# Kernel optimization log

Hardware: AMD Instinct MI355X
Metric: run time of the kernel (lower is better)

The kernel has to match this reference:

```python
import jax, jax.numpy as jnp
import numpy as np

EPS = 1e-5

def setup_inputs() -> dict:
    key = jax.random.key(0)
    ks = jax.random.split(key, 10)
    B, N, D = 1, 20000, 256
    E, H = 320000, 8
    s = 1.0 / np.sqrt(D)
    return {
        "node_embeddings": jax.random.normal(ks[0], (B, N, D), jnp.float32),
        "edge_index": jax.random.randint(ks[1], (2, E), 0, N, jnp.int32),
        "edge_weights": jax.random.uniform(ks[2], (E,), jnp.float32),
        "Wq": jax.random.normal(ks[3], (D, D), jnp.float32) * s,
        "Wk": jax.random.normal(ks[4], (D, D), jnp.float32) * s,
        "Wv": jax.random.normal(ks[5], (D, D), jnp.float32) * s,
        "We": jax.random.normal(ks[6], (H,), jnp.float32),  # edge_encoder weight [num_heads,1] squeezed
        "Wo": jax.random.normal(ks[7], (D, D), jnp.float32) * s,
        "ln_g": jnp.ones((D,), jnp.float32),
        "ln_b": jnp.zeros((D,), jnp.float32),
    }

def reference(node_embeddings, edge_index, edge_weights, Wq, Wk, Wv, We, Wo, ln_g, ln_b):
    B, N, D = node_embeddings.shape
    H = We.shape[0]
    hd = D // H
    scale = 1.0 / np.sqrt(hd)
    residual = node_embeddings

    # projections -> [B, N, H, hd]
    Q = (node_embeddings @ Wq).reshape(B, N, H, hd)
    K = (node_embeddings @ Wk).reshape(B, N, H, hd)
    V = (node_embeddings @ Wv).reshape(B, N, H, hd)

    src = edge_index[0]
    tgt = edge_index[1]
    E = src.shape[0]

    # gather per edge, edge axis leading for segment ops: [E, B, H, hd]
    Q_e = jnp.moveaxis(Q[:, src], 1, 0)
    K_e = jnp.moveaxis(K[:, tgt], 1, 0)
    V_e = jnp.moveaxis(V[:, tgt], 1, 0)

    # per-edge scores [E, B, H]
    scores = (Q_e * K_e).sum(-1) * scale
    bias = edge_weights[:, None] * We[None, :]            # [E, H]
    scores = scores + bias[:, None, :]

    # scatter softmax grouped by source node
    m = jax.ops.segment_max(scores, src, num_segments=N)   # [N, B, H]
    p = jnp.exp(scores - m[src])
    denom = jax.ops.segment_sum(p, src, num_segments=N)    # [N, B, H]
    attn = p / denom[src]                                   # [E, B, H]

    # scatter-add weighted V -> [N, B, H, hd]
    weighted = attn[..., None] * V_e
    agg = jax.ops.segment_sum(weighted.reshape(E, -1), src, num_segments=N)
    agg = agg.reshape(N, B, H, hd)

    attn_out = jnp.moveaxis(agg, 0, 1).reshape(B, N, D)     # [B, N, D]
    out = attn_out @ Wo

    x = out + residual
    mu = x.mean(-1, keepdims=True)
    var = ((x - mu) ** 2).mean(-1, keepdims=True)
    return (x - mu) / jnp.sqrt(var + EPS) * ln_g + ln_b
```

## Files before the change

### kernel.cpp

```cpp
#include <hip/hip_runtime.h>
#include <hip/hip_bf16.h>

typedef __attribute__((ext_vector_type(8))) short short8;
typedef __attribute__((ext_vector_type(4))) short short4_t;
typedef __attribute__((ext_vector_type(4))) float f32x4;

#define CH 64

__device__ __forceinline__ ushort f2b(float f) {
  __hip_bfloat16 h = __float2bfloat16(f);
  return *reinterpret_cast<ushort*>(&h);
}
__device__ __forceinline__ float b2f(ushort u) {
  return __uint_as_float(((unsigned)u) << 16);
}
__device__ __forceinline__ void wave_lds_sync() {
  asm volatile("s_waitcnt lgkmcnt(0)" ::: "memory");
  __builtin_amdgcn_wave_barrier();
}

__global__ __launch_bounds__(256) void pre_kernel(
    const float* __restrict__ Wq, const float* __restrict__ Wk,
    const float* __restrict__ Wv, const float* __restrict__ Wo,
    ushort* __restrict__ Wt, const int* __restrict__ src,
    int* __restrict__ counts, int E) {
  __shared__ float L[32][33];
  int b = blockIdx.x;
  int t = threadIdx.x;
  if (b < 256) {
    int mat = b >> 6;
    int tile = b & 63;
    int tr = (tile >> 3) * 32;
    int tc = (tile & 7) * 32;
    const float* W = (mat == 0) ? Wq : (mat == 1) ? Wk : (mat == 2) ? Wv : Wo;
    int c = t & 31, r8 = t >> 5;
#pragma unroll
    for (int rr = 0; rr < 4; ++rr) {
      int r = r8 + rr * 8;
      L[r][c] = W[(size_t)(tr + r) * 256 + tc + c];
    }
    __syncthreads();
#pragma unroll
    for (int rr = 0; rr < 4; ++rr) {
      int cc = r8 + rr * 8;
      Wt[(size_t)(mat * 256 + tc + cc) * 256 + tr + c] = f2b(L[c][cc]);
    }
  } else {
    int e = (b - 256) * 256 + t;
    if (e < E) atomicAdd(&counts[src[e]], 1);
  }
}

__global__ __launch_bounds__(256) void gemm_scan(
    const float* __restrict__ X, const ushort* __restrict__ Wt,
    ushort* __restrict__ QKVb, const int* __restrict__ counts,
    int* __restrict__ offs, int* __restrict__ cursor,
    int N, int ngemm) {
  __shared__ ushort sA[128 * 64];
  __shared__ ushort sB[128 * 64];
  __shared__ int wsum[4];
  __shared__ int wexc[4];
  __shared__ int s_total;
  int bid = blockIdx.x;
  int t = threadIdx.x;
  if (bid == ngemm) {
    int lane = t & 63, wv = t >> 6;
    int per = (N + 255) >> 8;
    int b0 = t * per;
    int e0 = min(b0 + per, N);
    int sum = 0;
    for (int i = b0; i < e0; ++i) sum += counts[i];
    int x = sum;
#pragma unroll
    for (int off = 1; off < 64; off <<= 1) {
      int y = __shfl_up(x, off);
      if (lane >= off) x += y;
    }
    if (lane == 63) wsum[wv] = x;
    __syncthreads();
    if (t == 0) {
      int run = 0;
#pragma unroll
      for (int k = 0; k < 4; ++k) { wexc[k] = run; run += wsum[k]; }
      s_total = run;
    }
    __syncthreads();
    int running = wexc[wv] + (x - sum);
    for (int i = b0; i < e0; ++i) {
      int c = counts[i];
      offs[i] = running;
      cursor[i] = running;
      running += c;
    }
    if (t == 0) offs[N] = s_total;
    return;
  }
  int bx = bid / 6, by = bid % 6;
  char* cA = (char*)sA;
  char* cB = (char*)sB;
  int lane = t & 63, w = t >> 6;
  int wr = w >> 1, wc = w & 1;
  int row0 = bx * 128;
  int lr = lane & 15, kg = lane >> 4;
  f32x4 acc[4][4] = {};
  for (int k0 = 0; k0 < 256; k0 += 64) {
#pragma unroll
    for (int it = 0; it < 4; ++it) {
      int slot = t + it * 256;
      int row = slot >> 3, kc = slot & 7;
      int grow = min(row0 + row, N - 1);
      const float* xp = X + (size_t)grow * 256 + k0 + kc * 8;
      float4 x0 = *reinterpret_cast<const float4*>(xp);
      float4 x1 = *reinterpret_cast<const float4*>(xp + 4);
      short8 va;
      va[0] = (short)f2b(x0.x); va[1] = (short)f2b(x0.y);
      va[2] = (short)f2b(x0.z); va[3] = (short)f2b(x0.w);
      va[4] = (short)f2b(x1.x); va[5] = (short)f2b(x1.y);
      va[6] = (short)f2b(x1.z); va[7] = (short)f2b(x1.w);
      *reinterpret_cast<short8*>(cA + ((row * 128 + kc * 16) ^ ((row & 7) << 4))) = va;
      short8 vb = *reinterpret_cast<const short8*>(Wt + (size_t)(by * 128 + row) * 256 + k0 + kc * 8);
      *reinterpret_cast<short8*>(cB + ((row * 128 + kc * 16) ^ ((row & 7) << 4))) = vb;
    }
    __syncthreads();
#pragma unroll
    for (int ks = 0; ks < 2; ++ks) {
      short8 af[4], bf[4];
#pragma unroll
      for (int fr = 0; fr < 4; ++fr) {
        int row = wr * 64 + fr * 16 + lr;
        af[fr] = *reinterpret_cast<const short8*>(
            cA + ((row * 128 + ks * 64 + kg * 16) ^ ((row & 7) << 4)));
      }
#pragma unroll
      for (int fc = 0; fc < 4; ++fc) {
        int col = wc * 64 + fc * 16 + lr;
        bf[fc] = *reinterpret_cast<const short8*>(
            cB + ((col * 128 + ks * 64 + kg * 16) ^ ((col & 7) << 4)));
      }
#pragma unroll
      for (int fr = 0; fr < 4; ++fr)
#pragma unroll
        for (int fc = 0; fc < 4; ++fc)
          acc[fr][fc] = __builtin_amdgcn_mfma_f32_16x16x32_bf16(af[fr], bf[fc], acc[fr][fc], 0, 0, 0);
    }
    __syncthreads();
  }
  int orow = kg * 4;
#pragma unroll
  for (int fr = 0; fr < 4; ++fr)
#pragma unroll
    for (int fc = 0; fc < 4; ++fc)
#pragma unroll
      for (int r = 0; r < 4; ++r) {
        int row = row0 + wr * 64 + fr * 16 + orow + r;
        int col = by * 128 + wc * 64 + fc * 16 + lr;
        if (row < N) QKVb[(size_t)row * 768 + col] = f2b(acc[fr][fc][r]);
      }
}

__global__ void scatter_kernel(const int* __restrict__ src, const int* __restrict__ tgt,
                               const float* __restrict__ ew, int* __restrict__ cursor,
                               int2* __restrict__ ews, int E) {
  int e = blockIdx.x * blockDim.x + threadIdx.x;
  if (e < E) {
    int pos = atomicAdd(&cursor[src[e]], 1);
    ews[pos] = make_int2(tgt[e], __float_as_int(ew[e]));
  }
}

__global__ __launch_bounds__(256) void attn_kernel(
    const ushort* __restrict__ QKVb,
    const int* __restrict__ offs, const int2* __restrict__ ews,
    const float* __restrict__ We, ushort* __restrict__ AGGb, int N) {
  __shared__ float s_p[4][CH][8];
  __shared__ int s_tgt[4][CH];
  __shared__ float s_w[4][CH];
  int t = threadIdx.x;
  int w = t >> 6;
  int l = t & 63;
  int i = blockIdx.x * 4 + w;
  if (i >= N) return;
  int e8 = l >> 3;
  int h = l & 7;
  int hacc = l >> 3;
  const float scale = 0.17677669529663687f;
  float we = We[h];

  float qf[32];
  {
    const short8* qr = reinterpret_cast<const short8*>(QKVb + (size_t)i * 768 + h * 32);
#pragma unroll
    for (int d = 0; d < 4; ++d) {
      short8 qv = qr[d];
#pragma unroll
      for (int x = 0; x < 8; ++x) qf[d * 8 + x] = b2f((ushort)qv[x]);
    }
  }

  float m = -1e30f, lsum = 0.f;
  float acc0 = 0.f, acc1 = 0.f, acc2 = 0.f, acc3 = 0.f;
  int beg = offs[i], end = offs[i + 1];

  for (int base = beg; base < end; base += CH) {
    int cnt = min(CH, end - base);
    int cnt_pad = (cnt + 7) & ~7;
    {
      bool valid = l < cnt;
      int2 te = valid ? ews[base + l] : make_int2(i, 0);
      s_tgt[w][l] = te.x;
      s_w[w][l] = valid ? __int_as_float(te.y) : 0.f;
    }
    wave_lds_sync();

    float s_local[8];
#pragma unroll
    for (int it = 0; it < 8; ++it) s_local[it] = -1e30f;

    short8 kc[4], kn[4];
    {
      const short8* p = reinterpret_cast<const short8*>(
          QKVb + (size_t)s_tgt[w][e8] * 768 + 256 + h * 32);
#pragma unroll
      for (int d = 0; d < 4; ++d) kc[d] = p[d];
    }
    if (8 < cnt_pad) {
      const short8* p = reinterpret_cast<const short8*>(
          QKVb + (size_t)s_tgt[w][8 + e8] * 768 + 256 + h * 32);
#pragma unroll
      for (int d = 0; d < 4; ++d) kn[d] = p[d];
    }
    float cmax = -1e30f;
#pragma unroll
    for (int it = 0; it < 8; ++it) {
      if (it * 8 >= cnt_pad) break;
      float dot = 0.f;
#pragma unroll
      for (int d = 0; d < 4; ++d)
#pragma unroll
        for (int x = 0; x < 8; ++x)
          dot += qf[d * 8 + x] * b2f((ushort)kc[d][x]);
      int j = it * 8 + e8;
      float s = (j < cnt) ? dot * scale + s_w[w][j] * we : -1e30f;
      s_local[it] = s;
      cmax = fmaxf(cmax, s);
#pragma unroll
      for (int d = 0; d < 4; ++d) kc[d] = kn[d];
      if ((it + 2) * 8 < cnt_pad) {
        const short8* p = reinterpret_cast<const short8*>(
            QKVb + (size_t)s_tgt[w][(it + 2) * 8 + e8] * 768 + 256 + h * 32);
#pragma unroll
        for (int d = 0; d < 4; ++d) kn[d] = p[d];
      }
    }
    cmax = fmaxf(cmax, __shfl_xor(cmax, 8));
    cmax = fmaxf(cmax, __shfl_xor(cmax, 16));
    cmax = fmaxf(cmax, __shfl_xor(cmax, 32));
    float newm = fmaxf(m, cmax);
    float f = __expf(m - newm);
    float psum = 0.f;
#pragma unroll
    for (int it = 0; it < 8; ++it) {
      if (it * 8 >= cnt_pad) break;
      int j = it * 8 + e8;
      float p = __expf(s_local[it] - newm);
      s_p[w][j][h] = p;
      psum += p;
    }
    psum += __shfl_xor(psum, 8);
    psum += __shfl_xor(psum, 16);
    psum += __shfl_xor(psum, 32);
    lsum = lsum * f + psum;
    m = newm;
    float f_acc = __shfl(f, hacc);
    acc0 *= f_acc; acc1 *= f_acc; acc2 *= f_acc; acc3 *= f_acc;
    wave_lds_sync();

#pragma unroll
    for (int g = 0; g < 8; ++g) {
      if (g * 8 >= cnt_pad) break;
      float pv[8];
      short4_t vv[8];
#pragma unroll
      for (int k = 0; k < 8; ++k) {
        int j = g * 8 + k;
        pv[k] = s_p[w][j][hacc];
        vv[k] = *reinterpret_cast<const short4_t*>(
            QKVb + (size_t)s_tgt[w][j] * 768 + 512 + l * 4);
      }
#pragma unroll
      for (int k = 0; k < 8; ++k) {
        acc0 += pv[k] * b2f((ushort)vv[k][0]);
        acc1 += pv[k] * b2f((ushort)vv[k][1]);
        acc2 += pv[k] * b2f((ushort)vv[k][2]);
        acc3 += pv[k] * b2f((ushort)vv[k][3]);
      }
    }
    wave_lds_sync();
  }
  float lsum_acc = __shfl(lsum, hacc);
  float rinv = (lsum_acc > 0.f) ? 1.f / lsum_acc : 0.f;
  short4_t o;
  o[0] = (short)f2b(acc0 * rinv);
  o[1] = (short)f2b(acc1 * rinv);
  o[2] = (short)f2b(acc2 * rinv);
  o[3] = (short)f2b(acc3 * rinv);
  *reinterpret_cast<short4_t*>(AGGb + (size_t)i * 256 + l * 4) = o;
}

__global__ __launch_bounds__(256) void out_ln(
    const ushort* __restrict__ AGGb, const ushort* __restrict__ Wot,
    const float* __restrict__ X, const float* __restrict__ g, const float* __restrict__ bb,
    float* __restrict__ out, int N) {
  __shared__ ushort sA[64 * 64];
  __shared__ ushort sB[256 * 64];
  char* cA = (char*)sA;
  char* cB = (char*)sB;
  int t = threadIdx.x;
  int lane = t & 63, w = t >> 6;
  int row0 = blockIdx.x * 64;
  int lr = lane & 15, kg = lane >> 4;
  f32x4 acc[16] = {};
  for (int k0 = 0; k0 < 256; k0 += 64) {
#pragma unroll
    for (int it = 0; it < 2; ++it) {
      int slot = t + it * 256;
      int row = slot >> 3, kc = slot & 7;
      int grow = min(row0 + row, N - 1);
      short8 va = *reinterpret_cast<const short8*>(AGGb + (size_t)grow * 256 + k0 + kc * 8);
      *reinterpret_cast<short8*>(cA + ((row * 128 + kc * 16) ^ ((row & 7) << 4))) = va;
    }
#pragma unroll
    for (int it = 0; it < 8; ++it) {
      int slot = t + it * 256;
      int col = slot >> 3, kc = slot & 7;
      short8 vb = *reinterpret_cast<const short8*>(Wot + (size_t)col * 256 + k0 + kc * 8);
      *reinterpret_cast<short8*>(cB + ((col * 128 + kc * 16) ^ ((col & 7) << 4))) = vb;
    }
    __syncthreads();
#pragma unroll
    for (int ks = 0; ks < 2; ++ks) {
      int arow = w * 16 + lr;
      short8 a = *reinterpret_cast<const short8*>(
          cA + ((arow * 128 + ks * 64 + kg * 16) ^ ((arow & 7) << 4)));
#pragma unroll
      for (int fc = 0; fc < 16; ++fc) {
        int col = fc * 16 + lr;
        short8 b = *reinterpret_cast<const short8*>(
            cB + ((col * 128 + ks * 64 + kg * 16) ^ ((col & 7) << 4)));
        acc[fc] = __builtin_amdgcn_mfma_f32_16x16x32_bf16(a, b, acc[fc], 0, 0, 0);
      }
    }
    __syncthreads();
  }
  float g16[16], b16[16];
#pragma unroll
  for (int fc = 0; fc < 16; ++fc) {
    g16[fc] = g[fc * 16 + lr];
    b16[fc] = bb[fc * 16 + lr];
  }
#pragma unroll
  for (int r = 0; r < 4; ++r) {
    int rowl = kg * 4 + r;
    int grow = row0 + w * 16 + rowl;
    int growc = min(grow, N - 1);
    float xv[16];
    float s = 0.f, ss = 0.f;
#pragma unroll
    for (int fc = 0; fc < 16; ++fc) {
      float v = acc[fc][r] + X[(size_t)growc * 256 + fc * 16 + lr];
      xv[fc] = v;
      s += v;
      ss += v * v;
    }
    s += __shfl_xor(s, 1);  ss += __shfl_xor(ss, 1);
    s += __shfl_xor(s, 2);  ss += __shfl_xor(ss, 2);
    s += __shfl_xor(s, 4);  ss += __shfl_xor(ss, 4);
    s += __shfl_xor(s, 8);  ss += __shfl_xor(ss, 8);
    float mu = s * (1.f / 256.f);
    float var = ss * (1.f / 256.f) - mu * mu;
    float rs = rsqrtf(var + 1e-5f);
    if (grow < N) {
#pragma unroll
      for (int fc = 0; fc < 16; ++fc)
        out[(size_t)grow * 256 + fc * 16 + lr] = (xv[fc] - mu) * rs * g16[fc] + b16[fc];
    }
  }
}

extern "C" void kernel_launch(void* const* d_in, const int* in_sizes, int n_in,
                              void* d_out, int out_size, void* d_ws, size_t ws_size,
                              hipStream_t stream) {
  const float* X  = (const float*)d_in[0];
  const int* eidx = (const int*)d_in[1];
  const float* ew = (const float*)d_in[2];
  const float* Wq = (const float*)d_in[3];
  const float* Wk = (const float*)d_in[4];
  const float* Wv = (const float*)d_in[5];
  const float* We = (const float*)d_in[6];
  const float* Wo = (const float*)d_in[7];
  const float* g  = (const float*)d_in[8];
  const float* b  = (const float*)d_in[9];
  int N = in_sizes[0] / 256;
  int E = in_sizes[1] / 2;
  const int* src = eidx;
  const int* tgt = eidx + E;
  float* out = (float*)d_out;

  char* w = (char*)d_ws;
  ushort* Wt   = (ushort*)w;  w += (size_t)1024 * 256 * 2;
  ushort* QKVb = (ushort*)w;  w += (size_t)N * 768 * 2;
  ushort* AGGb = (ushort*)w;  w += (size_t)N * 256 * 2;
  int* counts  = (int*)w;     w += (size_t)N * 4;
  int* offs    = (int*)w;     w += (size_t)(N + 1) * 4;
  int* cursor  = (int*)w;     w += (size_t)N * 4;
  int2* ews    = (int2*)w;    w += (size_t)E * 8;
  const ushort* Wot = Wt + (size_t)768 * 256;

  hipMemsetAsync(counts, 0, (size_t)N * 4, stream);

  int nhist = (E + 255) / 256;
  pre_kernel<<<256 + nhist, 256, 0, stream>>>(Wq, Wk, Wv, Wo, Wt, src, counts, E);

  int ngemm = ((N + 127) / 128) * 6;
  gemm_scan<<<ngemm + 1, 256, 0, stream>>>(X, Wt, QKVb, counts, offs, cursor, N, ngemm);

  scatter_kernel<<<(E + 255) / 256, 256, 0, stream>>>(src, tgt, ew, cursor, ews, E);
  attn_kernel<<<(N + 3) / 4, 256, 0, stream>>>(QKVb, offs, ews, We, AGGb, N);
  out_ln<<<(N + 63) / 64, 256, 0, stream>>>(AGGb, Wot, X, g, b, out, N);
}
```

Before: 172.7 us.

## Split scan from QKV GEMM, prefetch next K tile, remap workgroups per XCD

Moves the CSR offset scan out of the QKV GEMM into its own 1024-thread kernel, so the GEMM no longer carries a slow single-block straggler. Inside the GEMM, global loads for the next K-slice are issued into registers while the current slice's MFMAs run, overlapping memory latency with compute. Workgroup IDs are remapped so consecutive tiles land on the same XCD, which is meant to improve L2 reuse of the shared weight tiles. The cost is one extra kernel launch and higher register pressure from the prefetch buffers.

```diff
diff --git a/kernel.cpp b/kernel.cpp
--- a/kernel.cpp
+++ b/kernel.cpp
@@ -51,77 +51,64 @@
   }
 }
 
-__global__ __launch_bounds__(256) void gemm_scan(
+__global__ __launch_bounds__(256) void qkv_gemm(
     const float* __restrict__ X, const ushort* __restrict__ Wt,
-    ushort* __restrict__ QKVb, const int* __restrict__ counts,
-    int* __restrict__ offs, int* __restrict__ cursor,
-    int N, int ngemm) {
+    ushort* __restrict__ QKVb, int N) {
   __shared__ ushort sA[128 * 64];
   __shared__ ushort sB[128 * 64];
-  __shared__ int wsum[4];
-  __shared__ int wexc[4];
-  __shared__ int s_total;
-  int bid = blockIdx.x;
-  int t = threadIdx.x;
-  if (bid == ngemm) {
-    int lane = t & 63, wv = t >> 6;
-    int per = (N + 255) >> 8;
-    int b0 = t * per;
-    int e0 = min(b0 + per, N);
-    int sum = 0;
-    for (int i = b0; i < e0; ++i) sum += counts[i];
-    int x = sum;
-#pragma unroll
-    for (int off = 1; off < 64; off <<= 1) {
-      int y = __shfl_up(x, off);
-      if (lane >= off) x += y;
-    }
-    if (lane == 63) wsum[wv] = x;
-    __syncthreads();
-    if (t == 0) {
-      int run = 0;
-#pragma unroll
-      for (int k = 0; k < 4; ++k) { wexc[k] = run; run += wsum[k]; }
-      s_total = run;
-    }
-    __syncthreads();
-    int running = wexc[wv] + (x - sum);
-    for (int i = b0; i < e0; ++i) {
-      int c = counts[i];
-      offs[i] = running;
-      cursor[i] = running;
-      running += c;
-    }
-    if (t == 0) offs[N] = s_total;
-    return;
-  }
-  int bx = bid / 6, by = bid % 6;
   char* cA = (char*)sA;
   char* cB = (char*)sB;
+  int t = threadIdx.x;
+  int nwg = gridDim.x;
+  int o = blockIdx.x;
+  int q = nwg >> 3, r = nwg & 7;
+  int xcd = o & 7;
+  int wgid = (xcd < r ? xcd * (q + 1) : r * (q + 1) + (xcd - r) * q) + (o >> 3);
+  int bx = wgid / 6, by = wgid % 6;
   int lane = t & 63, w = t >> 6;
   int wr = w >> 1, wc = w & 1;
   int row0 = bx * 128;
   int lr = lane & 15, kg = lane >> 4;
+
+  int slotrow[4], slotkc[4], growv[4];
+#pragma unroll
+  for (int it = 0; it < 4; ++it) {
+    int slot = t + it * 256;
+    slotrow[it] = slot >> 3;
+    slotkc[it] = slot & 7;
+    growv[it] = min(row0 + slotrow[it], N - 1);
+  }
+
+  float4 px0[4], px1[4];
+  short8 pwb[4];
+#define ISSUE(K0)                                                                 \
+  {                                                                               \
+    _Pragma("unroll") for (int it = 0; it < 4; ++it) {                            \
+      const float* xp = X + (size_t)growv[it] * 256 + (K0) + slotkc[it] * 8;      \
+      px0[it] = *reinterpret_cast<const float4*>(xp);                             \
+      px1[it] = *reinterpret_cast<const float4*>(xp + 4);                         \
+      pwb[it] = *reinterpret_cast<const short8*>(                                 \
+          Wt + (size_t)(by * 128 + slotrow[it]) * 256 + (K0) + slotkc[it] * 8);   \
+    }                                                                             \
+  }
+
   f32x4 acc[4][4] = {};
+  ISSUE(0);
+#pragma unroll
   for (int k0 = 0; k0 < 256; k0 += 64) {
 #pragma unroll
     for (int it = 0; it < 4; ++it) {
-      int slot = t + it * 256;
-      int row = slot >> 3, kc = slot & 7;
-      int grow = min(row0 + row, N - 1);
-      const float* xp = X + (size_t)grow * 256 + k0 + kc * 8;
-      float4 x0 = *reinterpret_cast<const float4*>(xp);
-      float4 x1 = *reinterpret_cast<const float4*>(xp + 4);
       short8 va;
-      va[0] = (short)f2b(x0.x); va[1] = (short)f2b(x0.y);
-      va[2] = (short)f2b(x0.z); va[3] = (short)f2b(x0.w);
-      va[4] = (short)f2b(x1.x); va[5] = (short)f2b(x1.y);
-      va[6] = (short)f2b(x1.z); va[7] = (short)f2b(x1.w);
+      va[0] = (short)f2b(px0[it].x); va[1] = (short)f2b(px0[it].y);
+      va[2] = (short)f2b(px0[it].z); va[3] = (short)f2b(px0[it].w);
+      va[4] = (short)f2b(px1[it].x); va[5] = (short)f2b(px1[it].y);
+      va[6] = (short)f2b(px1[it].z); va[7] = (short)f2b(px1[it].w);
+      int row = slotrow[it], kc = slotkc[it];
       *reinterpret_cast<short8*>(cA + ((row * 128 + kc * 16) ^ ((row & 7) << 4))) = va;
-      short8 vb = *reinterpret_cast<const short8*>(Wt + (size_t)(by * 128 + row) * 256 + k0 + kc * 8);
-      *reinterpret_cast<short8*>(cB + ((row * 128 + kc * 16) ^ ((row & 7) << 4))) = vb;
+      *reinterpret_cast<short8*>(cB + ((row * 128 + kc * 16) ^ ((row & 7) << 4))) = pwb[it];
     }
     __syncthreads();
+    if (k0 < 192) ISSUE(k0 + 64);
 #pragma unroll
     for (int ks = 0; ks < 2; ++ks) {
       short8 af[4], bf[4];
@@ -145,17 +132,60 @@
     }
     __syncthreads();
   }
+#undef ISSUE
   int orow = kg * 4;
 #pragma unroll
   for (int fr = 0; fr < 4; ++fr)
 #pragma unroll
     for (int fc = 0; fc < 4; ++fc)
 #pragma unroll
-      for (int r = 0; r < 4; ++r) {
-        int row = row0 + wr * 64 + fr * 16 + orow + r;
+      for (int r2 = 0; r2 < 4; ++r2) {
+        int row = row0 + wr * 64 + fr * 16 + orow + r2;
         int col = by * 128 + wc * 64 + fc * 16 + lr;
-        if (row < N) QKVb[(size_t)row * 768 + col] = f2b(acc[fr][fc][r]);
-      }
+        if (row < N) QKVb[(size_t)row * 768 + col] = f2b(acc[fr][fc][r2]);
+      }
+}
+
+__global__ __launch_bounds__(1024) void scan_kernel(
+    const int* __restrict__ counts, int* __restrict__ offs, int* __restrict__ cursor, int N) {
+  __shared__ int wsum[16];
+  __shared__ int wexc[16];
+  __shared__ int s_total;
+  int t = threadIdx.x;
+  int lane = t & 63, wv = t >> 6;
+  int per = (N + 1023) >> 10;
+  int b0 = t * per;
+  int e0 = min(b0 + per, N);
+  int sum = 0;
+  for (int i = b0; i < e0; ++i) sum += counts[i];
+  int x = sum;
+#pragma unroll
+  for (int off = 1; off < 64; off <<= 1) {
+    int y = __shfl_up(x, off);
+    if (lane >= off) x += y;
+  }
+  if (lane == 63) wsum[wv] = x;
+  __syncthreads();
+  if (t < 64) {
+    int s = (lane < 16) ? wsum[lane] : 0;
+    int xs = s;
+#pragma unroll
+    for (int off = 1; off < 16; off <<= 1) {
+      int y = __shfl_up(xs, off);
+      if (lane >= off) xs += y;
+    }
+    if (lane < 16) wexc[lane] = xs - s;
+    if (lane == 15) s_total = xs;
+  }
+  __syncthreads();
+  int running = wexc[wv] + (x - sum);
+  for (int i = b0; i < e0; ++i) {
+    int c = counts[i];
+    offs[i] = running;
+    cursor[i] = running;
+    running += c;
+  }
+  if (t == 0) offs[N] = s_total;
 }
 
 __global__ void scatter_kernel(const int* __restrict__ src, const int* __restrict__ tgt,
@@ -422,8 +452,9 @@
   pre_kernel<<<256 + nhist, 256, 0, stream>>>(Wq, Wk, Wv, Wo, Wt, src, counts, E);
 
   int ngemm = ((N + 127) / 128) * 6;
-  gemm_scan<<<ngemm + 1, 256, 0, stream>>>(X, Wt, QKVb, counts, offs, cursor, N, ngemm);
-
+  qkv_gemm<<<ngemm, 256, 0, stream>>>(X, Wt, QKVb, N);
+
+  scan_kernel<<<1, 1024, 0, stream>>>(counts, offs, cursor, N);
   scatter_kernel<<<(E + 255) / 256, 256, 0, stream>>>(src, tgt, ew, cursor, ews, E);
   attn_kernel<<<(N + 3) / 4, 256, 0, stream>>>(QKVb, offs, ews, We, AGGb, N);
   out_ln<<<(N + 63) / 64, 256, 0, stream>>>(AGGb, Wot, X, g, b, out, N);
```

Measured after the change: 160.1 us. 1.08x faster.
